# Performance work log

Hardware: AMD Instinct MI355X
Metric: run time of the kernel (lower is better)

Reference implementation:

```python
import jax, jax.numpy as jnp
import numpy as np

K = 3          # kernel_size
H_BW = 0.5     # bandwidth 'h' in forward_chop


def _extract_patches(img, k):
    # Equivalent to F.conv2d(img, one_hot_kernel, stride=1, padding=0):
    # out channel index = c*k*k + ki*k + kj
    B, C, H, W = img.shape
    Ho, Wo = H - k + 1, W - k + 1
    sl = [img[:, :, i:i + Ho, j:j + Wo] for i in range(k) for j in range(k)]
    p = jnp.stack(sl, axis=2)                 # [B, C, k*k, Ho, Wo]
    return p.reshape(B, C * k * k, Ho, Wo)


def _pixel_shuffle(x, r):
    # torch F.pixel_shuffle: channel c*r*r + r1*r + r2 -> spatial (h*r+r1, w*r+r2)
    B, C, H, W = x.shape
    Co = C // (r * r)
    x = x.reshape(B, Co, r, r, H, W)
    x = x.transpose(0, 1, 4, 2, 5, 3)
    return x.reshape(B, Co, H * r, W * r)


def _overlap_add(patch, H, W, k, n_colors):
    # img_sum: strided pixel_shuffle overlap-add with ones-count normalization
    B = patch.shape[0]
    out = jnp.zeros((B, n_colors, H, W), patch.dtype)
    wei = jnp.zeros((1, 1, H, W), patch.dtype)
    ones = jnp.ones((1, k * k, patch.shape[2], patch.shape[3]), patch.dtype)
    for i in range(k):
        for j in range(k):
            px = _pixel_shuffle(patch[:, :, i::k, j::k], k)
            out = out.at[:, :, i:i + px.shape[2], j:j + px.shape[3]].add(px)
            wx = _pixel_shuffle(ones[:, :, i::k, j::k], k)
            wei = wei.at[:, :, i:i + wx.shape[2], j:j + wx.shape[3]].add(wx)
    return out / wei


def setup_inputs() -> dict:
    key = jax.random.key(0)
    kx, ky = jax.random.split(key)
    x = jax.random.normal(kx, (1, 3, 128, 128), dtype=jnp.float32)
    y = jax.random.normal(ky, (1, 3, 128, 128), dtype=jnp.float32)
    return {"x": x, "y": y}


def reference(x, y):
    # NonLocalModule.forward with h*w < min_size -> forward_chop(x, y)
    k = K
    B, C, H, W = x.shape
    ip = _extract_patches(x, k)               # [B, d, Ho, Wo], d = C*k*k
    rp = _extract_patches(y, k)
    d = ip.shape[1]
    L = ip.shape[2] * ip.shape[3]
    X = ip.reshape(B, d, L)                   # input patches  [B, d, L]
    XT = X.transpose(0, 2, 1)                 # [B, L, d]
    R = rp.reshape(B, d, L).transpose(0, 2, 1)  # refer patches [B, L, d]
    XY = jnp.einsum('bld,bdm->blm', R, X)     # [B, L, L]
    XX = jnp.sum(R * R, axis=2, keepdims=True)   # [B, L, 1]
    YY = jnp.sum(X * X, axis=1, keepdims=True)   # [B, 1, L]
    att = jax.nn.softmax((2.0 * XY - XX - YY) / (H_BW * H_BW + 0.1), axis=-1)
    out = jnp.einsum('blm,bmd->bld', att, XT)    # [B, L, d]
    out = out.transpose(0, 2, 1).reshape(ip.shape)
    return _overlap_add(out, H, W, k, C)
```

## Files before the change

### kernel.cpp

```cpp
#include <hip/hip_runtime.h>

#define LQv  15876
#define LP   16384
#define LQP  16384
#define HOc  126
#define NCH  16
#define C2L  8.243971662222648f
#define IC2L 0.1213006672795172f
#define CKS  4.121985831111324f

typedef __attribute__((ext_vector_type(8))) short bf16x8;
typedef __attribute__((ext_vector_type(4))) float f32x4;

#define MFMA(a,b,c) __builtin_amdgcn_mfma_f32_16x16x32_bf16((a),(b),(c),0,0,0)
#define EXP2(x) __builtin_amdgcn_exp2f(x)

__device__ __forceinline__ unsigned short f2bf_rne(float f) {
    unsigned u = __float_as_uint(f);
    unsigned r = ((u >> 16) & 1u) + 0x7FFFu;
    return (unsigned short)((u + r) >> 16);
}
__device__ __forceinline__ float bf2f(unsigned short h) {
    return __uint_as_float(((unsigned)h) << 16);
}
__device__ __forceinline__ void split_bf(float v, unsigned short& hi, unsigned short& lo) {
    hi = f2bf_rne(v);
    lo = f2bf_rne(v - bf2f(hi));
}
__device__ __forceinline__ constexpr int doffc(int d) {
    return (d / 9) * 16384 + ((d % 9) / 3) * 128 + ((d % 9) % 3);
}

__global__ __launch_bounds__(256) void prep_kernel(
    const float* __restrict__ x, const float* __restrict__ y,
    unsigned short* __restrict__ khi, unsigned short* __restrict__ klo,
    unsigned short* __restrict__ qhi, unsigned short* __restrict__ qlo,
    unsigned short* __restrict__ vt)
{
    int gidx = blockIdx.x * 256 + threadIdx.x;
    int pair = gidx >> 1, half = gidx & 1;
    int l = pair & (LP - 1);
    int role = pair >> 14;
    bool real = l < LQv;
    int i = real ? (l / HOc) : 0, j = real ? (l - i * HOc) : 0;
    int base = i * 128 + j;

    if (role < 2) {
        const float* __restrict__ src = role ? y : x;
        float scale = role ? C2L : 1.f;
        __align__(16) unsigned short hh[16], ll[16];
        float ss = 0.f;
#pragma unroll
        for (int it = 0; it < 16; ++it) {
            int offL = doffc(it);
            int offH = (16 + it < 27) ? doffc(16 + it) : 0;
            int off  = half ? offH : offL;
            bool ok  = (it < 11) ? real : (real && !half);
            float v = src[base + off];
            v = ok ? v : 0.f;
            ss = fmaf(v, v, ss);
            split_bf(scale * v, hh[it], ll[it]);
        }
        float tot = ss + __shfl_xor(ss, 1);
        if (half) {
            if (role == 0) {
                float ckv = real ? (-tot * CKS) : -1e30f;
                split_bf(ckv * IC2L, hh[11], ll[11]);
                hh[12] = ll[12] = 0;
                hh[13] = 0x3F80; ll[13] = 0;
                hh[14] = ll[14] = 0; hh[15] = ll[15] = 0;
            } else {
                split_bf(C2L, hh[11], ll[11]);
                hh[12] = ll[12] = 0;
                split_bf(80.f - CKS * tot, hh[13], ll[13]);
                hh[14] = ll[14] = 0; hh[15] = ll[15] = 0;
            }
        }
        int d0 = half << 4;
        unsigned short* dh = (role ? qhi : khi) + (size_t)l * 32 + d0;
        unsigned short* dl = (role ? qlo : klo) + (size_t)l * 32 + d0;
        ((uint4*)dh)[0] = ((uint4*)hh)[0]; ((uint4*)dh)[1] = ((uint4*)hh)[1];
        ((uint4*)dl)[0] = ((uint4*)ll)[0]; ((uint4*)dl)[1] = ((uint4*)ll)[1];
    } else {
        int kap = l & 31;
        int cp = 8 * ((kap >> 2) & 3) + 4 * (kap >> 4) + (kap & 3);
        int lp = (l & ~31) | cp;
        unsigned short* vbase = vt + lp + (half ? 16 * LP : 0);
#pragma unroll
        for (int it = 0; it < 16; ++it) {
            int offL = doffc(it);
            int offH = (16 + it < 27) ? doffc(16 + it) : 0;
            int off  = half ? offH : offL;
            bool ok  = (it < 11) ? real : (real && !half);
            float xv = x[base + off];
            unsigned short v;
            if (it == 11)
                v = ok ? f2bf_rne(xv) : ((real && half) ? (unsigned short)0x3F80
                                                        : (unsigned short)0);
            else
                v = ok ? f2bf_rne(xv) : 0;
            vbase[it * LP] = v;
        }
    }
}

__global__ __launch_bounds__(256, 4) void attn_kernel(
    const unsigned short* __restrict__ khi, const unsigned short* __restrict__ klo,
    const unsigned short* __restrict__ qhi, const unsigned short* __restrict__ qlo,
    const unsigned short* __restrict__ vt,  unsigned int* __restrict__ opart)
{
    int lane = threadIdx.x & 63;
    int wave = threadIdx.x >> 6;
    int n = lane & 15, g = lane >> 4;
    int qb = blockIdx.x * 256 + wave * 64;
    int ch = blockIdx.y;

    bf16x8 bqh[4], bql[4];
#pragma unroll
    for (int t = 0; t < 4; ++t) {
        bqh[t] = *(const bf16x8*)(qhi + (size_t)(qb + t * 16 + n) * 32 + g * 8);
        bql[t] = *(const bf16x8*)(qlo + (size_t)(qb + t * 16 + n) * 32 + g * 8);
    }

    f32x4 o0[4], o1[4];
#pragma unroll
    for (int t = 0; t < 4; ++t) {
        o0[t] = (f32x4){0.f, 0.f, 0.f, 0.f};
        o1[t] = (f32x4){0.f, 0.f, 0.f, 0.f};
    }

    int kb0 = ch * 1024;
    for (int it = 0; it < 32; ++it) {
        int kb = kb0 + it * 32;
        bf16x8 akh0 = *(const bf16x8*)(khi + (size_t)(kb + n) * 32 + g * 8);
        bf16x8 akl0 = *(const bf16x8*)(klo + (size_t)(kb + n) * 32 + g * 8);
        bf16x8 akh1 = *(const bf16x8*)(khi + (size_t)(kb + 16 + n) * 32 + g * 8);
        bf16x8 akl1 = *(const bf16x8*)(klo + (size_t)(kb + 16 + n) * 32 + g * 8);
        bf16x8 v0 = *(const bf16x8*)(vt + (size_t)n * LP + kb + g * 8);
        bf16x8 v1 = *(const bf16x8*)(vt + (size_t)(16 + n) * LP + kb + g * 8);
#pragma unroll
        for (int qt = 0; qt < 4; ++qt) {
            f32x4 cc0 = {0.f, 0.f, 0.f, 0.f}, cc1 = {0.f, 0.f, 0.f, 0.f};
            cc0 = MFMA(akh0, bqh[qt], cc0); cc1 = MFMA(akh1, bqh[qt], cc1);
            cc0 = MFMA(akh0, bql[qt], cc0); cc1 = MFMA(akh1, bql[qt], cc1);
            cc0 = MFMA(akl0, bqh[qt], cc0); cc1 = MFMA(akl1, bqh[qt], cc1);
            float p0 = EXP2(cc0[0]);
            float p1 = EXP2(cc0[1]);
            float p2 = EXP2(cc0[2]);
            float p3 = EXP2(cc0[3]);
            float p4 = EXP2(cc1[0]);
            float p5 = EXP2(cc1[1]);
            float p6 = EXP2(cc1[2]);
            float p7 = EXP2(cc1[3]);
            union { unsigned u[4]; bf16x8 v; } ap;
            ap.u[0] = __builtin_amdgcn_perm(__float_as_uint(p1), __float_as_uint(p0), 0x07060302u);
            ap.u[1] = __builtin_amdgcn_perm(__float_as_uint(p3), __float_as_uint(p2), 0x07060302u);
            ap.u[2] = __builtin_amdgcn_perm(__float_as_uint(p5), __float_as_uint(p4), 0x07060302u);
            ap.u[3] = __builtin_amdgcn_perm(__float_as_uint(p7), __float_as_uint(p6), 0x07060302u);
            o0[qt] = MFMA(ap.v, v0, o0[qt]);
            o1[qt] = MFMA(ap.v, v1, o1[qt]);
        }
    }

#pragma unroll
    for (int qt = 0; qt < 4; ++qt) {
#pragma unroll
        for (int r = 0; r < 4; ++r) {
            unsigned w = ((unsigned)f2bf_rne(o1[qt][r]) << 16) | f2bf_rne(o0[qt][r]);
            size_t row = (size_t)ch * LQP + qb + qt * 16 + 4 * g + r;
            opart[row * 16 + n] = w;
        }
    }
}

__global__ __launch_bounds__(256) void final_kernel(
    const unsigned int* __restrict__ opart, float* __restrict__ out)
{
    __shared__ float lpatch[100 * 32];
    int tid = threadIdx.x;
    int lane = tid & 63;
    int h0 = (blockIdx.x >> 4) * 8, w0 = (blockIdx.x & 15) * 8;

    for (int t = tid; t < 1600; t += 256) {
        int rr = t >> 4, n = t & 15;
        int di = rr / 10, dj = rr - di * 10;
        int I = h0 - 2 + di, J = w0 - 2 + dj;
        bool valid = ((unsigned)I < 126u) && ((unsigned)J < 126u);
        int l = valid ? (I * HOc + J) : 0;
        float s0 = 0.f, s1 = 0.f;
#pragma unroll
        for (int c = 0; c < NCH; ++c) {
            unsigned v = opart[((size_t)c * LQP + l) * 16 + n];
            s0 += bf2f((unsigned short)(v & 0xffffu));
            s1 += bf2f((unsigned short)(v >> 16));
        }
        float denom = __shfl(s1, (lane & 48) | 11);
        float inv = 1.f / denom;
        lpatch[rr * 32 + n]      = s0 * inv;
        lpatch[rr * 32 + 16 + n] = s1 * inv;
    }
    __syncthreads();

    if (tid < 192) {
        int c = tid >> 6, pix = tid & 63;
        int h = h0 + (pix >> 3), w = w0 + (pix & 7);
        float sum = 0.f; int cnt = 0;
#pragma unroll
        for (int r1 = 0; r1 < 3; ++r1) {
            int I = h - r1; if ((unsigned)I >= 126u) continue;
#pragma unroll
            for (int r2 = 0; r2 < 3; ++r2) {
                int J = w - r2; if ((unsigned)J >= 126u) continue;
                int rr = (I - (h0 - 2)) * 10 + (J - (w0 - 2));
                sum += lpatch[rr * 32 + c * 9 + r1 * 3 + r2];
                ++cnt;
            }
        }
        out[c * 16384 + h * 128 + w] = sum / (float)cnt;
    }
}

extern "C" void kernel_launch(void* const* d_in, const int* in_sizes, int n_in,
                              void* d_out, int out_size, void* d_ws, size_t ws_size,
                              hipStream_t stream)
{
    const float* x = (const float*)d_in[0];
    const float* y = (const float*)d_in[1];
    float* out = (float*)d_out;

    unsigned short* khi = (unsigned short*)d_ws;
    unsigned short* klo = khi + (size_t)LP * 32;
    unsigned short* qhi = klo + (size_t)LP * 32;
    unsigned short* qlo = qhi + (size_t)LQP * 32;
    unsigned short* vt  = qlo + (size_t)LQP * 32;
    unsigned int* opart = (unsigned int*)(vt + (size_t)32 * LP);

    dim3 blk(256);
    prep_kernel <<<dim3(384),     blk, 0, stream>>>(x, y, khi, klo, qhi, qlo, vt);
    attn_kernel <<<dim3(64, NCH), blk, 0, stream>>>(khi, klo, qhi, qlo, vt, opart);
    final_kernel<<<dim3(256),     blk, 0, stream>>>(opart, out);
}
```

Measured before the change: 134.0 us.

## Double-buffer K/V tiles in LDS via async global_load_lds prefetch

Result: faster. 121.3 us (-9.5%).

```diff
diff --git a/kernel.cpp b/kernel.cpp
--- a/kernel.cpp
+++ b/kernel.cpp
@@ -104,11 +104,19 @@
     }
 }
 
+__device__ __forceinline__ void gload16(const unsigned short* g, unsigned short* l)
+{
+    __builtin_amdgcn_global_load_lds(
+        (__attribute__((address_space(1))) void*)g,
+        (__attribute__((address_space(3))) void*)l, 16, 0, 0);
+}
+
 __global__ __launch_bounds__(256, 4) void attn_kernel(
     const unsigned short* __restrict__ khi, const unsigned short* __restrict__ klo,
     const unsigned short* __restrict__ qhi, const unsigned short* __restrict__ qlo,
     const unsigned short* __restrict__ vt,  unsigned int* __restrict__ opart)
 {
+    __shared__ __align__(16) unsigned short lds[2][3072];
     int lane = threadIdx.x & 63;
     int wave = threadIdx.x >> 6;
     int n = lane & 15, g = lane >> 4;
@@ -130,20 +138,45 @@
     }
 
     int kb0 = ch * 1024;
+
+#define STAGE(dst, kb) do {                                                   \
+        if (wave == 0) {                                                      \
+            gload16(khi + (size_t)(kb) * 32 + lane * 8,       (dst));         \
+            gload16(khi + (size_t)(kb) * 32 + 512 + lane * 8, (dst) + 512);   \
+        } else if (wave == 1) {                                               \
+            gload16(klo + (size_t)(kb) * 32 + lane * 8,       (dst) + 1024);  \
+            gload16(klo + (size_t)(kb) * 32 + 512 + lane * 8, (dst) + 1536);  \
+        } else if (wave == 2) {                                               \
+            gload16(vt + (size_t)(lane >> 2) * LP + (kb) + (lane & 3) * 8,    \
+                    (dst) + 2048);                                            \
+        } else {                                                              \
+            gload16(vt + (size_t)(16 + (lane >> 2)) * LP + (kb) + (lane & 3) * 8, \
+                    (dst) + 2560);                                            \
+        }                                                                     \
+    } while (0)
+
+    STAGE(lds[0], kb0);
+    __syncthreads();
+
+    int buf = 0;
     for (int it = 0; it < 32; ++it) {
-        int kb = kb0 + it * 32;
-        bf16x8 akh0 = *(const bf16x8*)(khi + (size_t)(kb + n) * 32 + g * 8);
-        bf16x8 akl0 = *(const bf16x8*)(klo + (size_t)(kb + n) * 32 + g * 8);
-        bf16x8 akh1 = *(const bf16x8*)(khi + (size_t)(kb + 16 + n) * 32 + g * 8);
-        bf16x8 akl1 = *(const bf16x8*)(klo + (size_t)(kb + 16 + n) * 32 + g * 8);
-        bf16x8 v0 = *(const bf16x8*)(vt + (size_t)n * LP + kb + g * 8);
-        bf16x8 v1 = *(const bf16x8*)(vt + (size_t)(16 + n) * LP + kb + g * 8);
+        int kbn = kb0 + ((it + 1) & 31) * 32;
+        STAGE(lds[buf ^ 1], kbn);
+
+        const unsigned short* L = lds[buf];
+        bf16x8 kh0 = *(const bf16x8*)(L + n * 32 + g * 8);
+        bf16x8 kh1 = *(const bf16x8*)(L + (16 + n) * 32 + g * 8);
+        bf16x8 kl0 = *(const bf16x8*)(L + 1024 + n * 32 + g * 8);
+        bf16x8 kl1 = *(const bf16x8*)(L + 1024 + (16 + n) * 32 + g * 8);
+        bf16x8 v0  = *(const bf16x8*)(L + 2048 + n * 32 + g * 8);
+        bf16x8 v1  = *(const bf16x8*)(L + 2048 + (16 + n) * 32 + g * 8);
+
 #pragma unroll
         for (int qt = 0; qt < 4; ++qt) {
             f32x4 cc0 = {0.f, 0.f, 0.f, 0.f}, cc1 = {0.f, 0.f, 0.f, 0.f};
-            cc0 = MFMA(akh0, bqh[qt], cc0); cc1 = MFMA(akh1, bqh[qt], cc1);
-            cc0 = MFMA(akh0, bql[qt], cc0); cc1 = MFMA(akh1, bql[qt], cc1);
-            cc0 = MFMA(akl0, bqh[qt], cc0); cc1 = MFMA(akl1, bqh[qt], cc1);
+            cc0 = MFMA(kh0, bqh[qt], cc0); cc1 = MFMA(kh1, bqh[qt], cc1);
+            cc0 = MFMA(kh0, bql[qt], cc0); cc1 = MFMA(kh1, bql[qt], cc1);
+            cc0 = MFMA(kl0, bqh[qt], cc0); cc1 = MFMA(kl1, bqh[qt], cc1);
             float p0 = EXP2(cc0[0]);
             float p1 = EXP2(cc0[1]);
             float p2 = EXP2(cc0[2]);
@@ -160,7 +193,10 @@
             o0[qt] = MFMA(ap.v, v0, o0[qt]);
             o1[qt] = MFMA(ap.v, v1, o1[qt]);
         }
-    }
+        __syncthreads();
+        buf ^= 1;
+    }
+#undef STAGE
 
 #pragma unroll
     for (int qt = 0; qt < 4; ++qt) {
```

## Double-buffer K/V tiles in LDS via async global_load_lds per wave

Applied to the files above, without the earlier changes.

New measurement: 126.7 us. 1.06x faster.

```diff
diff --git a/kernel.cpp b/kernel.cpp
--- a/kernel.cpp
+++ b/kernel.cpp
@@ -104,14 +104,26 @@
     }
 }
 
-__global__ __launch_bounds__(256, 4) void attn_kernel(
+__device__ __forceinline__ void gload16(const unsigned short* g, unsigned short* l)
+{
+    __builtin_amdgcn_global_load_lds(
+        (__attribute__((address_space(1))) void*)g,
+        (__attribute__((address_space(3))) void*)l, 16, 0, 0);
+}
+
+#define SLANE8(lane) ((((lane) & ~3) | (((lane) & 3) ^ (((lane) >> 3) & 3))) * 8)
+#define SCHUNK8(lane) ((((lane) & 3) ^ (((lane) >> 3) & 3)) * 8)
+
+__global__ __launch_bounds__(256, 3) void attn_kernel(
     const unsigned short* __restrict__ khi, const unsigned short* __restrict__ klo,
     const unsigned short* __restrict__ qhi, const unsigned short* __restrict__ qlo,
     const unsigned short* __restrict__ vt,  unsigned int* __restrict__ opart)
 {
+    __shared__ __align__(16) unsigned short lds[4][2][3072];
     int lane = threadIdx.x & 63;
     int wave = threadIdx.x >> 6;
     int n = lane & 15, g = lane >> 4;
+    int gx = g ^ ((n >> 1) & 3);
     int qb = blockIdx.x * 256 + wave * 64;
     int ch = blockIdx.y;
 
@@ -130,20 +142,43 @@
     }
 
     int kb0 = ch * 1024;
+
+#define STAGE_W(dst, kb) do {                                                 \
+        gload16(khi + (size_t)(kb) * 32 +       SLANE8(lane), (dst));         \
+        gload16(khi + (size_t)(kb) * 32 + 512 + SLANE8(lane), (dst) + 512);   \
+        gload16(klo + (size_t)(kb) * 32 +       SLANE8(lane), (dst) + 1024);  \
+        gload16(klo + (size_t)(kb) * 32 + 512 + SLANE8(lane), (dst) + 1536);  \
+        gload16(vt + (size_t)(lane >> 2) * LP + (kb) + SCHUNK8(lane),         \
+                (dst) + 2048);                                                \
+        gload16(vt + (size_t)(16 + (lane >> 2)) * LP + (kb) + SCHUNK8(lane),  \
+                (dst) + 2560);                                                \
+    } while (0)
+
+    unsigned short* W0 = lds[wave][0];
+    unsigned short* W1 = lds[wave][1];
+
+    STAGE_W(W0, kb0);
     for (int it = 0; it < 32; ++it) {
-        int kb = kb0 + it * 32;
-        bf16x8 akh0 = *(const bf16x8*)(khi + (size_t)(kb + n) * 32 + g * 8);
-        bf16x8 akl0 = *(const bf16x8*)(klo + (size_t)(kb + n) * 32 + g * 8);
-        bf16x8 akh1 = *(const bf16x8*)(khi + (size_t)(kb + 16 + n) * 32 + g * 8);
-        bf16x8 akl1 = *(const bf16x8*)(klo + (size_t)(kb + 16 + n) * 32 + g * 8);
-        bf16x8 v0 = *(const bf16x8*)(vt + (size_t)n * LP + kb + g * 8);
-        bf16x8 v1 = *(const bf16x8*)(vt + (size_t)(16 + n) * LP + kb + g * 8);
+        int kbn = kb0 + ((it + 1) & 31) * 32;
+        unsigned short* cur = (it & 1) ? W1 : W0;
+        unsigned short* nxt = (it & 1) ? W0 : W1;
+        STAGE_W(nxt, kbn);
+        asm volatile("s_waitcnt vmcnt(6)" ::: "memory");
+        __builtin_amdgcn_sched_barrier(0);
+
+        bf16x8 kh0 = *(const bf16x8*)(cur + n * 32 + gx * 8);
+        bf16x8 kh1 = *(const bf16x8*)(cur + (16 + n) * 32 + gx * 8);
+        bf16x8 kl0 = *(const bf16x8*)(cur + 1024 + n * 32 + gx * 8);
+        bf16x8 kl1 = *(const bf16x8*)(cur + 1024 + (16 + n) * 32 + gx * 8);
+        bf16x8 v0  = *(const bf16x8*)(cur + 2048 + n * 32 + gx * 8);
+        bf16x8 v1  = *(const bf16x8*)(cur + 2048 + (16 + n) * 32 + gx * 8);
+
 #pragma unroll
         for (int qt = 0; qt < 4; ++qt) {
             f32x4 cc0 = {0.f, 0.f, 0.f, 0.f}, cc1 = {0.f, 0.f, 0.f, 0.f};
-            cc0 = MFMA(akh0, bqh[qt], cc0); cc1 = MFMA(akh1, bqh[qt], cc1);
-            cc0 = MFMA(akh0, bql[qt], cc0); cc1 = MFMA(akh1, bql[qt], cc1);
-            cc0 = MFMA(akl0, bqh[qt], cc0); cc1 = MFMA(akl1, bqh[qt], cc1);
+            cc0 = MFMA(kh0, bqh[qt], cc0); cc1 = MFMA(kh1, bqh[qt], cc1);
+            cc0 = MFMA(kh0, bql[qt], cc0); cc1 = MFMA(kh1, bql[qt], cc1);
+            cc0 = MFMA(kl0, bqh[qt], cc0); cc1 = MFMA(kl1, bqh[qt], cc1);
             float p0 = EXP2(cc0[0]);
             float p1 = EXP2(cc0[1]);
             float p2 = EXP2(cc0[2]);
@@ -161,6 +196,7 @@
             o1[qt] = MFMA(ap.v, v1, o1[qt]);
         }
     }
+#undef STAGE_W
 
 #pragma unroll
     for (int qt = 0; qt < 4; ++qt) {
```
